# Kernel optimization log

Hardware: AMD Instinct MI355X
Metric: run time of the kernel (lower is better)

## Reference

```python
import jax, jax.numpy as jnp
import numpy as np

B, T, NT = 2, 2048, 512
DIM, DEPTH, MEL, TDIM = 768, 8, 100, 512
D_INNER, NS, PH, Q = 1536, 128, 64, 64
NH = D_INNER // PH
CONV_DIM = D_INNER + 2 * NS
D_INPROJ = 2 * D_INNER + 2 * NS + NH
KCONV = 4
FFI = 2 * DIM
VOCAB = 257


def _ln(x, eps=1e-6):
    m = jnp.mean(x, -1, keepdims=True)
    v = jnp.mean((x - m) ** 2, -1, keepdims=True)
    return (x - m) * jax.lax.rsqrt(v + eps)


def _mish(x):
    return x * jnp.tanh(jax.nn.softplus(x))


def _dwconv_causal(x, w, b):
    # x: [B,T,C], w: [C,K]  depthwise causal conv (left-pad K-1)
    K = w.shape[1]
    xp = jnp.pad(x, ((0, 0), (K - 1, 0), (0, 0)))
    y = sum(xp[:, k:k + x.shape[1]] * w[:, k] for k in range(K))
    return y + b


def _ssd(xh, Bm, Cm, dt, A):
    # chunked selective-scan (Mamba SSD form). xh [B,T,H,P]; Bm,Cm [B,T,N]; dt [B,T,H]; A [H]
    Bsz, Tt, H, P = xh.shape
    N = Bm.shape[-1]
    Cn = Tt // Q
    xb = (dt[..., None] * xh).reshape(Bsz, Cn, Q, H, P)
    a = (dt * A).reshape(Bsz, Cn, Q, H)
    Bc = Bm.reshape(Bsz, Cn, Q, N)
    Cc = Cm.reshape(Bsz, Cn, Q, N)
    acum = jnp.cumsum(a, axis=2)  # [b,c,q,h]
    # intra-chunk: decay matrix exp(acum_q - acum_s) for s <= q
    Ldec = jnp.exp(acum[:, :, :, None, :] - acum[:, :, None, :, :])  # [b,c,q,s,h]
    mask = jnp.tril(jnp.ones((Q, Q), dtype=bool))
    Ldec = jnp.where(mask[None, None, :, :, None], Ldec, 0.0)
    CB = jnp.einsum('bcqn,bcsn->bcqs', Cc, Bc)
    y_in = jnp.einsum('bcqs,bcqsh,bcshp->bcqhp', CB, Ldec, xb)
    # chunk end-states
    dst = jnp.exp(acum[:, :, -1:, :] - acum)  # [b,c,q,h]
    S = jnp.einsum('bcqh,bcqn,bcqhp->bchpn', dst, Bc, xb)
    atot = jnp.exp(acum[:, :, -1, :])  # [b,c,h] total chunk decay

    def step(Hc, inp):
        at_c, S_c = inp
        return at_c[:, :, None, None] * Hc + S_c, Hc

    H0 = jnp.zeros((Bsz, H, P, N), xh.dtype)
    _, prev = jax.lax.scan(step, H0, (jnp.moveaxis(atot, 1, 0), jnp.moveaxis(S, 1, 0)))
    prev = jnp.moveaxis(prev, 0, 1)  # state entering each chunk [b,c,h,p,n]
    y_out = jnp.einsum('bcqn,bchpn->bcqhp', Cc, prev) * jnp.exp(acum)[..., None]
    return (y_in + y_out).reshape(Bsz, Tt, H, P)


def _forward(x, cond, time, text, text_table, inp_w, inp_b, pos_w1, pos_b1, pos_w2, pos_b2, t_w1, t_b1, t_w2, t_b2, adaln_w, adaln_b, in_w, conv_w, conv_b, dt_bias, A_log, Dp, rms_w, out_w, ff_w1, ff_b1, ff_w2, ff_b2, fin_w, fin_b, proj_w, proj_b):
    # timestep embedding (sinusoidal, scale 1000, freq dim 256 -> MLP)
    half = 128
    freqs = jnp.exp(-jnp.log(10000.0) / (half - 1) * jnp.arange(half, dtype=x.dtype))
    ang = 1000.0 * time[:, None] * freqs[None]
    te = jnp.concatenate([jnp.sin(ang), jnp.cos(ang)], -1)
    tvec = jax.nn.silu(te @ t_w1 + t_b1) @ t_w2 + t_b2  # [B,DIM]
    # text embedding (conv_layers=0 path): shift by 1, pad to seq_len, lookup
    idx = jnp.pad(text + 1, ((0, 0), (0, T - text.shape[1])))
    temb = text_table[idx]  # [B,T,TDIM]
    # input embedding + ConvPositionEmbedding (grouped conv k=31, groups=16, Mish x2)
    h = jnp.concatenate([x, cond, temb], -1) @ inp_w + inp_b  # [B,T,DIM]
    dn = ('NWC', 'WIO', 'NWC')
    p = jax.lax.conv_general_dilated(h, pos_w1, (1,), [(15, 15)], dimension_numbers=dn, feature_group_count=16) + pos_b1
    p = _mish(p)
    p = jax.lax.conv_general_dilated(p, pos_w2, (1,), [(15, 15)], dimension_numbers=dn, feature_group_count=16) + pos_b2
    h = h + _mish(p)
    st = jax.nn.silu(tvec)
    for l in range(DEPTH):
        mod = st @ adaln_w[l] + adaln_b[l]
        sh_msa, sc_msa, g_msa, sh_mlp, sc_mlp, g_mlp = jnp.split(mod, 6, -1)
        xn = _ln(h) * (1 + sc_msa[:, None]) + sh_msa[:, None]
        # Mamba-3 selective scan block
        zxbcdt = xn @ in_w[l]
        z = zxbcdt[..., :D_INNER]
        xBC = zxbcdt[..., D_INNER:D_INNER + CONV_DIM]
        dt = zxbcdt[..., D_INNER + CONV_DIM:]
        xBC = jax.nn.silu(_dwconv_causal(xBC, conv_w[l], conv_b[l]))
        xp = xBC[..., :D_INNER].reshape(B, T, NH, PH)
        Bm = xBC[..., D_INNER:D_INNER + NS]
        Cm = xBC[..., D_INNER + NS:]
        dt = jax.nn.softplus(dt + dt_bias[l])
        A = -jnp.exp(A_log[l])
        y = _ssd(xp, Bm, Cm, dt, A) + Dp[l][:, None] * xp
        y = y.reshape(B, T, D_INNER) * jax.nn.silu(z)
        y = y * jax.lax.rsqrt(jnp.mean(y * y, -1, keepdims=True) + 1e-5) * rms_w[l]
        h = h + g_msa[:, None] * (y @ out_w[l])
        # gated FFN
        xn = _ln(h) * (1 + sc_mlp[:, None]) + sh_mlp[:, None]
        ff = jax.nn.gelu(xn @ ff_w1[l] + ff_b1[l], approximate=True) @ ff_w2[l] + ff_b2[l]
        h = h + g_mlp[:, None] * ff
    fm = st @ fin_w + fin_b
    sc, sh = jnp.split(fm, 2, -1)
    h = _ln(h) * (1 + sc[:, None]) + sh[:, None]
    return h @ proj_w + proj_b


def setup_inputs() -> dict:
    key = jax.random.key(0)
    it = iter(jax.random.split(key, 40))

    def n(shape, s=0.02):
        return (s * jax.random.normal(next(it), shape)).astype(jnp.float32)

    inp = {
        'x': n((B, T, MEL), 1.0),
        'cond': n((B, T, MEL), 1.0),
        'time': jax.random.uniform(next(it), (B,), dtype=jnp.float32),
        'text_table': n((VOCAB, TDIM)),
        'inp_w': n((2 * MEL + TDIM, DIM)), 'inp_b': jnp.zeros((DIM,), jnp.float32),
        'pos_w1': n((31, DIM // 16, DIM), 0.05), 'pos_b1': jnp.zeros((DIM,), jnp.float32),
        'pos_w2': n((31, DIM // 16, DIM), 0.05), 'pos_b2': jnp.zeros((DIM,), jnp.float32),
        't_w1': n((256, DIM)), 't_b1': jnp.zeros((DIM,), jnp.float32),
        't_w2': n((DIM, DIM)), 't_b2': jnp.zeros((DIM,), jnp.float32),
        'adaln_w': n((DEPTH, DIM, 6 * DIM)), 'adaln_b': jnp.zeros((DEPTH, 6 * DIM), jnp.float32),
        'in_w': n((DEPTH, DIM, D_INPROJ)),
        'conv_w': n((DEPTH, CONV_DIM, KCONV), 0.2), 'conv_b': jnp.zeros((DEPTH, CONV_DIM), jnp.float32),
        'dt_bias': n((DEPTH, NH), 0.5),
        'A_log': jnp.log(jnp.tile(jnp.arange(1, NH + 1, dtype=jnp.float32), (DEPTH, 1))),
        'Dp': jnp.ones((DEPTH, NH), jnp.float32),
        'rms_w': jnp.ones((DEPTH, D_INNER), jnp.float32),
        'out_w': n((DEPTH, D_INNER, DIM)),
        'ff_w1': n((DEPTH, DIM, FFI)), 'ff_b1': jnp.zeros((DEPTH, FFI), jnp.float32),
        'ff_w2': n((DEPTH, FFI, DIM)), 'ff_b2': jnp.zeros((DEPTH, DIM), jnp.float32),
        'fin_w': n((DIM, 2 * DIM)), 'fin_b': jnp.zeros((2 * DIM,), jnp.float32),
        'proj_w': n((DIM, MEL)), 'proj_b': jnp.zeros((MEL,), jnp.float32),
    }
    inp['text'] = jax.random.randint(next(it), (B, NT), 0, 256)
    return inp


def reference(x, cond, time, text, text_table, inp_w, inp_b, pos_w1, pos_b1, pos_w2, pos_b2, t_w1, t_b1, t_w2, t_b2, adaln_w, adaln_b, in_w, conv_w, conv_b, dt_bias, A_log, Dp, rms_w, out_w, ff_w1, ff_b1, ff_w2, ff_b2, fin_w, fin_b, proj_w, proj_b):
    return _forward(x, cond, time, text, text_table, inp_w, inp_b, pos_w1, pos_b1, pos_w2, pos_b2, t_w1, t_b1, t_w2, t_b2, adaln_w, adaln_b, in_w, conv_w, conv_b, dt_bias, A_log, Dp, rms_w, out_w, ff_w1, ff_b1, ff_w2, ff_b2, fin_w, fin_b, proj_w, proj_b)
```

## Files before the change

kernel.cpp:

```cpp
#include <hip/hip_runtime.h>
#include <math.h>

constexpr int Bv = 2, Tv = 2048, NTv = 512;
constexpr int DIMv = 768, DEPTHv = 8, MELv = 100, TDIMv = 512;
constexpr int DINNER = 1536, NSv = 128, PHv = 64, QQv = 64;
constexpr int NHv = DINNER / PHv;
constexpr int CONVD = DINNER + 2 * NSv;
constexpr int DINP = 2 * DINNER + 2 * NSv + NHv;
constexpr int KCONVv = 4, FFIv = 2 * DIMv;
constexpr int CNv = Tv / QQv;
constexpr int PCK = 1504;
constexpr int KCAT = 736;

typedef unsigned short u16;
typedef unsigned int u32;
typedef __attribute__((ext_vector_type(8))) short short8v;
typedef __attribute__((ext_vector_type(4))) float f32x4;

__device__ __forceinline__ float siluf(float x) { return x / (1.f + expf(-x)); }
__device__ __forceinline__ float softplusf(float x) { return x > 20.f ? x : log1pf(expf(x)); }
__device__ __forceinline__ float mishf(float x) { return x * tanhf(softplusf(x)); }

__device__ __forceinline__ u16 f2bf(float v) {
    u32 u = __builtin_bit_cast(u32, v);
    u32 r = (u + 0x7fffu + ((u >> 16) & 1u)) >> 16;
    return (u16)r;
}
__device__ __forceinline__ float bf2f(u16 v) {
    u32 u = (u32)v << 16;
    return __builtin_bit_cast(float, u);
}
__device__ __forceinline__ float bf2fs(short v) { return bf2f((u16)v); }

__device__ __forceinline__ void gload16(const void* g, void* l) {
    __builtin_amdgcn_global_load_lds(
        (const __attribute__((address_space(1))) u32*)g,
        (__attribute__((address_space(3))) u32*)l, 16, 0, 0);
}

__device__ __forceinline__ float blockReduceSum(float v) {
    __shared__ float red[4];
    #pragma unroll
    for (int off = 32; off > 0; off >>= 1) v += __shfl_down(v, off, 64);
    __syncthreads();
    if ((threadIdx.x & 63) == 0) red[threadIdx.x >> 6] = v;
    __syncthreads();
    return red[0] + red[1] + red[2] + red[3];
}

template <int EPI, int BIG>
__global__ __launch_bounds__(256) void gemm_bf16(const u16* __restrict__ A,
        const u16* __restrict__ BT, const float* __restrict__ bias,
        float* __restrict__ Cf, u16* __restrict__ Cb,
        int M, int N, int K, int ldc,
        const float* __restrict__ modv, int goff, int mstride) {
    constexpr int BM = BIG ? 128 : 64;
    constexpr int MI = 4;
    constexpr int NJ = BIG ? 4 : 2;
    __shared__ __align__(16) u16 As[2][BM * 32];
    __shared__ __align__(16) u16 Bs[2][128 * 32];
    const int tid = threadIdx.x;
    const int gx = gridDim.x;
    const int nwg = gx * gridDim.y;
    int flat = blockIdx.y * gx + blockIdx.x;
    const int qq = nwg >> 3;
    flat = (flat & 7) * qq + (flat >> 3);
    const int m0 = (flat / gx) * BM, n0 = (flat % gx) * 128;
    const int lane = tid & 63;
    const int wid = tid >> 6;
    const int wm = BIG ? (wid >> 1) * 64 : 0;
    const int wn = BIG ? (wid & 1) * 64 : wid * 32;
    f32x4 acc[MI][NJ] = {};
    const int srow = tid >> 2, sseg = (tid & 3) * 8;
    const u16* Ag = A + (size_t)(m0 + srow) * K + sseg;
    const u16* Bg = BT + (size_t)(n0 + srow) * K + sseg;
    const int lr = lane & 15, lk = (lane >> 4) * 8;
    gload16(Ag, &As[0][tid * 8]);
    if (BIG) gload16(Ag + (size_t)64 * K, &As[0][tid * 8 + 64 * 32]);
    gload16(Bg, &Bs[0][tid * 8]);
    gload16(Bg + (size_t)64 * K, &Bs[0][tid * 8 + 64 * 32]);
    __syncthreads();
    int cur = 0;
    for (int k0 = 0; k0 < K; k0 += 32) {
        if (k0 + 32 < K) {
            const int nb = cur ^ 1, kn = k0 + 32;
            gload16(Ag + kn, &As[nb][tid * 8]);
            if (BIG) gload16(Ag + kn + (size_t)64 * K, &As[nb][tid * 8 + 64 * 32]);
            gload16(Bg + kn, &Bs[nb][tid * 8]);
            gload16(Bg + kn + (size_t)64 * K, &Bs[nb][tid * 8 + 64 * 32]);
        }
        short8v a_f[MI], b_f[NJ];
        #pragma unroll
        for (int i = 0; i < MI; i++)
            a_f[i] = *(const short8v*)&As[cur][(wm + i * 16 + lr) * 32 + lk];
        #pragma unroll
        for (int j = 0; j < NJ; j++)
            b_f[j] = *(const short8v*)&Bs[cur][(wn + j * 16 + lr) * 32 + lk];
        #pragma unroll
        for (int i = 0; i < MI; i++)
            #pragma unroll
            for (int j = 0; j < NJ; j++)
                acc[i][j] = __builtin_amdgcn_mfma_f32_16x16x32_bf16(a_f[i], b_f[j], acc[i][j], 0, 0, 0);
        __syncthreads();
        cur ^= 1;
    }
    const int r0 = (lane >> 4) * 4;
    #pragma unroll
    for (int i = 0; i < MI; i++) {
        #pragma unroll
        for (int j = 0; j < NJ; j++) {
            const int col = n0 + wn + j * 16 + lr;
            if (col >= N) continue;
            const int row = m0 + wm + i * 16 + r0;
            const float bv = (EPI == 1 || EPI == 2 || EPI == 4) ? bias[col] : 0.f;
            #pragma unroll
            for (int r = 0; r < 4; r++) {
                float v = acc[i][j][r] + bv;
                if (EPI == 0) {
                    Cb[(size_t)(row + r) * ldc + col] = f2bf(v);
                } else if (EPI == 2) {
                    float xx = v;
                    v = 0.5f * xx * (1.f + tanhf(0.7978845608028654f * (xx + 0.044715f * xx * xx * xx)));
                    Cb[(size_t)(row + r) * ldc + col] = f2bf(v);
                } else if (EPI == 3 || EPI == 4) {
                    const int bb = (row + r) >> 11;
                    float g = modv[(size_t)bb * mstride + goff + col];
                    Cf[(size_t)(row + r) * ldc + col] += g * v;
                } else {
                    Cf[(size_t)(row + r) * ldc + col] = v;
                }
            }
        }
    }
}

__global__ __launch_bounds__(256) void wt_convert_b(const float* __restrict__ W,
        u16* __restrict__ WT, int Kd, int N, int Kmax, int Npad) {
    const float* Wl = W + (size_t)blockIdx.z * Kmax * N;
    u16* WTl = WT + (size_t)blockIdx.z * Npad * Kd;
    __shared__ float t[32][33];
    const int n0 = blockIdx.x * 32, k0 = blockIdx.y * 32;
    const int c = threadIdx.x & 31, rq = (threadIdx.x >> 5) * 4;
    #pragma unroll
    for (int i = 0; i < 4; i++) {
        int n = n0 + c, k = k0 + rq + i;
        t[rq + i][c] = (n < N && k < Kmax) ? Wl[(size_t)k * N + n] : 0.f;
    }
    __syncthreads();
    #pragma unroll
    for (int i = 0; i < 4; i++)
        WTl[(size_t)(n0 + rq + i) * Kd + k0 + c] = f2bf(t[c][rq + i]);
}

__global__ __launch_bounds__(256) void pw_convert(const float* __restrict__ w,
        u16* __restrict__ WT) {
    __shared__ float t[32][33];
    const int kk0 = blockIdx.x * 32, o0 = blockIdx.y * 32;
    const int c = threadIdx.x & 31, rq = (threadIdx.x >> 5) * 4;
    #pragma unroll
    for (int i = 0; i < 4; i++) {
        int kk = kk0 + rq + i;
        t[rq + i][c] = (kk < 1488) ? w[(size_t)kk * DIMv + o0 + c] : 0.f;
    }
    __syncthreads();
    #pragma unroll
    for (int i = 0; i < 4; i++)
        WT[(size_t)(o0 + rq + i) * PCK + kk0 + c] = f2bf(t[c][rq + i]);
}

template <int IN_BF, int FUSE>
__global__ __launch_bounds__(256) void posconv_mfma(const void* __restrict__ inv,
        const u16* __restrict__ WT, const float* __restrict__ bias,
        void* __restrict__ outv) {
    __shared__ __align__(16) u16 xs[95 * 48];
    const int t0 = blockIdx.x * 64, g = blockIdx.y, b = blockIdx.z;
    const int tid = threadIdx.x;
    for (int e = tid; e < 95 * 48; e += 256) {
        int rr = e / 48, cc = e % 48;
        int t = t0 - 15 + rr;
        float v = 0.f;
        if (t >= 0 && t < Tv) {
            size_t gi = ((size_t)b * Tv + t) * DIMv + g * 48 + cc;
            v = IN_BF ? bf2f(((const u16*)inv)[gi]) : ((const float*)inv)[gi];
        }
        xs[e] = f2bf(v);
    }
    __syncthreads();
    const int lane = tid & 63, w = tid >> 6;
    const int lr = lane & 15, lq8 = (lane >> 4) * 8, rq = (lane >> 4) * 4;
    const u16* arow = &xs[(w * 16 + lr) * 48 + lq8];
    const u16* brow = &WT[(size_t)(g * 48 + lr) * PCK + lq8];
    f32x4 acc[3] = {};
    #pragma unroll 2
    for (int ks = 0; ks < PCK / 32; ks++) {
        short8v a = *(const short8v*)(arow + ks * 32);
        #pragma unroll
        for (int j = 0; j < 3; j++) {
            short8v bf = *(const short8v*)(brow + (size_t)j * 16 * PCK + ks * 32);
            acc[j] = __builtin_amdgcn_mfma_f32_16x16x32_bf16(a, bf, acc[j], 0, 0, 0);
        }
    }
    #pragma unroll
    for (int j = 0; j < 3; j++) {
        const int o = g * 48 + j * 16 + lr;
        const float bvv = bias[o];
        #pragma unroll
        for (int r = 0; r < 4; r++) {
            const int t = t0 + w * 16 + rq + r;
            float v = acc[j][r] + bvv;
            size_t gi = ((size_t)b * Tv + t) * DIMv + o;
            if (FUSE == 0) ((u16*)outv)[gi] = f2bf(mishf(v));
            else ((float*)outv)[gi] += mishf(v);
        }
    }
}

// ... 31 lines not shown
    const int o = blockIdx.x * 64 + (threadIdx.x & 63);
    const int ks = threadIdx.x >> 6;
    __shared__ float hv[DIMv];
    __shared__ float part[4][64];
    for (int j = threadIdx.x; j < DIMv; j += 256) hv[j] = hid[b * DIMv + j];
    __syncthreads();
    float acc = 0.f;
    #pragma unroll 8
    for (int k = ks * 192; k < ks * 192 + 192; k++) acc += hv[k] * t_w2[(size_t)k * DIMv + o];
    part[ks][threadIdx.x & 63] = acc;
    __syncthreads();
    if (threadIdx.x < 64) {
        float r = part[0][threadIdx.x] + part[1][threadIdx.x] + part[2][threadIdx.x] + part[3][threadIdx.x]
                + t_b2[o];
        st_out[b * DIMv + o] = siluf(r);
    }
}

__global__ __launch_bounds__(256) void modvec_kernel(const float* __restrict__ st,
        const float* __restrict__ W, const float* __restrict__ bias,
        float* __restrict__ out, int N) {
    const int l = blockIdx.z, b = blockIdx.y;
    const int o = blockIdx.x * 64 + (threadIdx.x & 63);
    const int ks = threadIdx.x >> 6;
    __shared__ float sv[DIMv];
    __shared__ float part[4][64];
    for (int j = threadIdx.x; j < DIMv; j += 256) sv[j] = st[b * DIMv + j];
    __syncthreads();
    const float* Wl = W + (size_t)l * DIMv * N + o;
    float acc = 0.f;
    #pragma unroll 8
    for (int k = ks * 192; k < ks * 192 + 192; k++) acc += sv[k] * Wl[(size_t)k * N];
    part[ks][threadIdx.x & 63] = acc;
    __syncthreads();
    if (threadIdx.x < 64) {
        float r = part[0][threadIdx.x] + part[1][threadIdx.x] + part[2][threadIdx.x] + part[3][threadIdx.x]
                + bias[(size_t)l * N + o];
        out[((size_t)l * Bv + b) * N + o] = r;
    }
}

__global__ void concat_bf16(const float* __restrict__ x, const float* __restrict__ cond,
                            const float* __restrict__ table, const int* __restrict__ text,
                            u16* __restrict__ cat) {
    size_t i = (size_t)blockIdx.x * 256 + threadIdx.x;
    const size_t total = (size_t)Bv * Tv * KCAT;
    if (i >= total) return;
    int j = (int)(i % KCAT);
    size_t row = i / KCAT;
    int t = (int)(row % Tv), b = (int)(row / Tv);
    float v = 0.f;
    if (j < MELv) v = x[row * MELv + j];
    else if (j < 2 * MELv) v = cond[row * MELv + (j - MELv)];
    else if (j < 712) {
        int idx = (t < NTv) ? (text[b * NTv + t] + 1) : 0;
        v = table[(size_t)idx * TDIMv + (j - 2 * MELv)];
    }
    cat[i] = f2bf(v);
}

template <int BF>
__global__ __launch_bounds__(256) void ln_mod_kernel(const float* __restrict__ h,
        void* __restrict__ outv, const float* __restrict__ modv,
        int sc_off, int sh_off, int mod_stride) {
    const int row = blockIdx.x;
    const int b = row / Tv;
    const float* hr = h + (size_t)row * DIMv;
    float s = 0.f;
    for (int j = threadIdx.x; j < DIMv; j += 256) s += hr[j];
    s = blockReduceSum(s);
    const float m = s / DIMv;
    float v = 0.f;
    for (int j = threadIdx.x; j < DIMv; j += 256) { float d = hr[j] - m; v += d * d; }
    v = blockReduceSum(v);
    const float rstd = rsqrtf(v / DIMv + 1e-6f);
    const float* mb = modv + (size_t)b * mod_stride;
    for (int j = threadIdx.x; j < DIMv; j += 256) {
        float val = (hr[j] - m) * rstd * (1.f + mb[sc_off + j]) + mb[sh_off + j];
        if (BF) ((u16*)outv)[(size_t)row * DIMv + j] = f2bf(val);
        else ((float*)outv)[(size_t)row * DIMv + j] = val;
    }
}

__global__ void dwconv_bc(const u16* __restrict__ zxb, const float* __restrict__ cw,
                          const float* __restrict__ cb, u16* __restrict__ xbcBC) {
    size_t i = (size_t)blockIdx.x * 256 + threadIdx.x;
    const size_t total = (size_t)Bv * Tv * 32;
    if (i >= total) return;
    const int c8 = (int)(i & 31) * 8;
    const size_t row = i >> 5;
    const int t = (int)(row % Tv);
    const u16* base = zxb + row * DINP + DINNER + c8;
    float acc[8];
    #pragma unroll
    for (int u = 0; u < 8; u++) acc[u] = cb[DINNER + c8 + u];
    #pragma unroll
    for (int k = 0; k < KCONVv; k++) {
        const int d = k - 3;
        if (t + d < 0) continue;
        short8v tv = *(const short8v*)(base + (ptrdiff_t)d * DINP);
        #pragma unroll
        for (int u = 0; u < 8; u++)
            acc[u] += bf2fs(tv[u]) * cw[(DINNER + c8 + u) * KCONVv + k];
    }
    short8v outv;
    #pragma unroll
    for (int u = 0; u < 8; u++) outv[u] = (short)f2bf(siluf(acc[u]));
    *(short8v*)(xbcBC + row * 256 + c8) = outv;
}

__global__ __launch_bounds__(256) void dwconvT(const u16* __restrict__ zxb,
        const float* __restrict__ cw, const float* __restrict__ cb,
        u16* __restrict__ xT) {
    __shared__ __align__(16) u16 in_s[67 * 72];
    const int pb = blockIdx.x;
    const int c = blockIdx.y, b = blockIdx.z;
    const int bc = b * CNv + c;
    const int tid = threadIdx.x;
    for (int e = tid; e < 67 * 8; e += 256) {
        int sp = e >> 3, p8 = (e & 7) * 8;
        int t = c * 64 + sp - 3;
        short8v v = {};
        if (t >= 0)
            v = *(const short8v*)&zxb[((size_t)b * Tv + t) * DINP + DINNER + pb * 64 + p8];
        *(short8v*)&in_s[sp * 72 + p8] = v;
    }
    __syncthreads();
    const int p = tid >> 2, sb = (tid & 3) * 16;
    const int ch = pb * 64 + p;
    const float w0 = cw[ch * 4], w1 = cw[ch * 4 + 1], w2 = cw[ch * 4 + 2], w3 = cw[ch * 4 + 3];
    const float bb = cb[ch];
    short8v o0, o1;
    #pragma unroll
    for (int i = 0; i < 16; i++) {
        int s = sb + i;
        float acc = bb + bf2f(in_s[s * 72 + p]) * w0 + bf2f(in_s[(s + 1) * 72 + p]) * w1
                  + bf2f(in_s[(s + 2) * 72 + p]) * w2 + bf2f(in_s[(s + 3) * 72 + p]) * w3;
        short r = (short)f2bf(siluf(acc));
        if (i < 8) o0[i] = r; else o1[i - 8] = r;
    }
    u16* dst = xT + ((size_t)bc * DINNER + ch) * 64 + sb;
    *(short8v*)dst = o0;
    *(short8v*)(dst + 8) = o1;
}

__global__ __launch_bounds__(256) void ssd_cb(const u16* __restrict__ xbcBC,
        float* __restrict__ CBg, u16* __restrict__ BTg) {
    constexpr int ST = 136;
    __shared__ __align__(16) u16 Cs[64 * ST];
    __shared__ __align__(16) u16 Bs[64 * ST];
    const int c = blockIdx.x, b = blockIdx.y;
    const int bc = b * CNv + c;
    const int tid = threadIdx.x;
    const size_t rowbase = (size_t)b * Tv + (size_t)c * QQv;
    for (int e = tid; e < 64 * 16; e += 256) {
        int r = e >> 4, n8 = (e & 15) * 8;
        const u16* src = &xbcBC[(rowbase + r) * 256];
        *(short8v*)&Bs[r * ST + n8] = *(const short8v*)(src + n8);
        *(short8v*)&Cs[r * ST + n8] = *(const short8v*)(src + NSv + n8);
    }
    __syncthreads();
    u16* btg = BTg + (size_t)bc * (NSv * QQv);
    for (int e = tid; e < 128 * 64; e += 256) {
        int n = e >> 6, s = e & 63;
        btg[e] = Bs[s * ST + n];
    }
    const int lane = tid & 63, w = tid >> 6;
    const int lr = lane & 15, lk8 = (lane >> 4) * 8, rq = (lane >> 4) * 4;
    f32x4 acc[4] = {};
    #pragma unroll
    for (int ks = 0; ks < 4; ks++) {
        short8v a = *(const short8v*)&Cs[(w * 16 + lr) * ST + ks * 32 + lk8];
        #pragma unroll
        for (int j = 0; j < 4; j++) {
            short8v bf = *(const short8v*)&Bs[(j * 16 + lr) * ST + ks * 32 + lk8];
            acc[j] = __builtin_amdgcn_mfma_f32_16x16x32_bf16(a, bf, acc[j], 0, 0, 0);
        }
    }
    float* out = CBg + (size_t)bc * 4096;
    #pragma unroll
    for (int j = 0; j < 4; j++)
        #pragma unroll
        for (int r = 0; r < 4; r++)
            out[(w * 16 + rq + r) * 64 + j * 16 + lr] = acc[j][r];
}

__global__ __launch_bounds__(256) void ssd_part1m(const u16* __restrict__ xT,
        const u16* __restrict__ BTg, const u16* __restrict__ zxb,
        const float* __restrict__ dt_bias, const float* __restrict__ A_log,
        const float* __restrict__ CBg, u16* __restrict__ ybuf,
        float* __restrict__ Sg, float* __restrict__ acg, float* __restrict__ atg) {
    constexpr int ST64 = 72;
    __shared__ __align__(16) u16 xTs[64 * ST64];
    __shared__ __align__(16) u16 Wsm[64 * ST64];
    __shared__ __align__(16) u16 BTs[128 * ST64];
    __shared__ float ac[64], dts[64], dtrev[64];
    const int h = blockIdx.x, c = blockIdx.y, b = blockIdx.z;
    const int bc = b * CNv + c;
    const int tid = threadIdx.x;
    const size_t rowbase = (size_t)b * Tv + (size_t)c * QQv;
    const size_t bch = ((size_t)bc) * NHv + h;
    if (tid < 64) {
        float raw = bf2f(zxb[(rowbase + tid) * DINP + DINNER + CONVD + h]) + dt_bias[h];
        float dtv = softplusf(raw);
        dts[tid] = dtv;
        float v = dtv * (-expf(A_log[h]));
        #pragma unroll
        for (int off = 1; off < 64; off <<= 1) {
            float t = __shfl_up(v, off, 64);
            if (tid >= off) v += t;
        }
        ac[tid] = v;
        float v63 = __shfl(v, 63, 64);
        dtrev[tid] = dtv * expf(v63 - v);
        acg[bch * 64 + tid] = v;
        if (tid == 63) atg[bch] = expf(v63);
    }
    {
        const u16* src = xT + ((size_t)bc * DINNER + h * PHv) * 64;
        for (int e = tid; e < 64 * 8; e += 256) {
            int p = e >> 3, s8 = (e & 7) * 8;
            *(short8v*)&xTs[p * ST64 + s8] = *(const short8v*)(src + p * 64 + s8);
        }
    }
    __syncthreads();
    {
        const u16* btg = BTg + (size_t)bc * (NSv * QQv);
        for (int e = tid; e < 128 * 8; e += 256) {
            int n = e >> 3, s8 = (e & 7) * 8;
            short8v v = *(const short8v*)(btg + n * 64 + s8);
            short8v o;
            #pragma unroll
            for (int u = 0; u < 8; u++)
                o[u] = (short)f2bf(bf2fs(v[u]) * dtrev[s8 + u]);
            *(short8v*)&BTs[n * ST64 + s8] = o;
        }
        const float* cbrow = CBg + (size_t)bc * 4096;
        for (int e = tid; e < 1024; e += 256) {
            int q = e >> 4, s4 = (e & 15) * 4;
            f32x4 cb4 = *(const f32x4*)&cbrow[q * 64 + s4];
            float aq = ac[q];
            #pragma unroll
            for (int u = 0; u < 4; u++) {
                int s = s4 + u;
                float wv = (s <= q) ? cb4[u] * expf(aq - ac[s]) * dts[s] : 0.f;
                Wsm[q * ST64 + s] = f2bf(wv);
            }
        }
    }
    __syncthreads();
    const int lane = tid & 63, w = tid >> 6;
    const int lr = lane & 15, lk8 = (lane >> 4) * 8, rq = (lane >> 4) * 4;
    {
        f32x4 acc[4] = {};
        #pragma unroll
        for (int ks = 0; ks < 2; ks++) {
            short8v bf = *(const short8v*)&xTs[(w * 16 + lr) * ST64 + ks * 32 + lk8];
            #pragma unroll
            for (int i = 0; i < 4; i++) {
                short8v a = *(const short8v*)&Wsm[(i * 16 + lr) * ST64 + ks * 32 + lk8];
                acc[i] = __builtin_amdgcn_mfma_f32_16x16x32_bf16(a, bf, acc[i], 0, 0, 0);
            }
        }
        #pragma unroll
        for (int i = 0; i < 4; i++)
            #pragma unroll
            for (int r = 0; r < 4; r++) {
                int q = i * 16 + rq + r, p = w * 16 + lr;
                ybuf[(rowbase + q) * DINNER + h * PHv + p] = f2bf(acc[i][r]);
            }
    }
    {
        f32x4 acc[4][2] = {};
        #pragma unroll
        for (int ks = 0; ks < 2; ks++) {
            short8v a[4];
            #pragma unroll
            for (int i = 0; i < 4; i++)
                a[i] = *(const short8v*)&xTs[(i * 16 + lr) * ST64 + ks * 32 + lk8];
            #pragma unroll
            for (int j = 0; j < 2; j++) {
                short8v bf = *(const short8v*)&BTs[(w * 32 + j * 16 + lr) * ST64 + ks * 32 + lk8];
                #pragma unroll
                for (int i = 0; i < 4; i++)
                    acc[i][j] = __builtin_amdgcn_mfma_f32_16x16x32_bf16(a[i], bf, acc[i][j], 0, 0, 0);
            }
        }
        float* So = Sg + bch * (PHv * NSv);
        #pragma unroll
        for (int i = 0; i < 4; i++)
            #pragma unroll
            for (int j = 0; j < 2; j++)
                #pragma unroll
                for (int r = 0; r < 4; r++)
                    So[(i * 16 + rq + r) * NSv + w * 32 + j * 16 + lr] = acc[i][j][r];
    }
}

__global__ void ssd_scan(float* __restrict__ Sg, const float* __restrict__ atg) {
    int idx = blockIdx.x * 256 + threadIdx.x;
    if (idx >= Bv * NHv * PHv * NSv) return;
    int n = idx % NSv;
    int p = (idx / NSv) % PHv;
    int h = (idx / (NSv * PHv)) % NHv;
    int b = idx / (NSv * PHv * NHv);
    float H = 0.f;
    for (int c = 0; c < CNv; c++) {
        size_t bch = ((size_t)b * CNv + c) * NHv + h;
        size_t off = bch * PHv * NSv + (size_t)p * NSv + n;
        float s = Sg[off];
        float at = atg[bch];
        Sg[off] = H;
        H = at * H + s;
    }
}

__global__ __launch_bounds__(256) void ssd_part2m(const u16* __restrict__ xbcBC,
        const u16* __restrict__ xT, const float* __restrict__ Sg,
        const float* __restrict__ acg, const float* __restrict__ Dp,
        u16* __restrict__ ybuf) {
    constexpr int ST = 136;
    __shared__ __align__(16) u16 Cs[64 * ST];
    __shared__ __align__(16) u16 Ps[64 * ST];
    __shared__ float eac[64];
    const int h = blockIdx.x, c = blockIdx.y, b = blockIdx.z;
    const int bc = b * CNv + c;
    const int tid = threadIdx.x;
    const size_t rowbase = (size_t)b * Tv + (size_t)c * QQv;
    const size_t bch = ((size_t)bc) * NHv + h;
    if (tid < 64) eac[tid] = expf(acg[bch * 64 + tid]);
    for (int e = tid; e < 64 * 16; e += 256) {
        int r = e >> 4, n8 = (e & 15) * 8;
        *(short8v*)&Cs[r * ST + n8] =
            *(const short8v*)&xbcBC[(rowbase + r) * 256 + NSv + n8];
        const float* src = &Sg[bch * (PHv * NSv) + (size_t)r * NSv + n8];
        f32x4 a = *(const f32x4*)src, b4 = *(const f32x4*)(src + 4);
        short8v o;
        o[0] = (short)f2bf(a[0]); o[1] = (short)f2bf(a[1]);
        o[2] = (short)f2bf(a[2]); o[3] = (short)f2bf(a[3]);
        o[4] = (short)f2bf(b4[0]); o[5] = (short)f2bf(b4[1]);
        o[6] = (short)f2bf(b4[2]); o[7] = (short)f2bf(b4[3]);
        *(short8v*)&Ps[r * ST + n8] = o;
    }
    __syncthreads();
    const int lane = tid & 63, w = tid >> 6;
    const int lr = lane & 15, lk8 = (lane >> 4) * 8, rq = (lane >> 4) * 4;
    f32x4 acc[4] = {};
    #pragma unroll
    for (int ks = 0; ks < 4; ks++) {
        short8v bf = *(const short8v*)&Ps[(w * 16 + lr) * ST + ks * 32 + lk8];
        #pragma unroll
        for (int i = 0; i < 4; i++) {
            short8v a = *(const short8v*)&Cs[(i * 16 + lr) * ST + ks * 32 + lk8];
            acc[i] = __builtin_amdgcn_mfma_f32_16x16x32_bf16(a, bf, acc[i], 0, 0, 0);
        }
    }
    const float Dh = Dp[h];
    const int p = w * 16 + lr;
    const u16* xrow = xT + ((size_t)bc * DINNER + h * PHv + p) * 64;
    #pragma unroll
    for (int i = 0; i < 4; i++)
        #pragma unroll
        for (int r = 0; r < 4; r++) {
            int q = i * 16 + rq + r;
            size_t yi = (rowbase + q) * DINNER + h * PHv + p;
            float xv = bf2f(xrow[q]);
            ybuf[yi] = f2bf(bf2f(ybuf[yi]) + acc[i][r] * eac[q] + Dh * xv);
        }
}

__global__ __launch_bounds__(256) void gate_rms_kernel(const u16* __restrict__ y,
        const u16* __restrict__ zxb, const float* __restrict__ rms_w,
        u16* __restrict__ yb) {
    const int row = blockIdx.x;
    const u16* yr = y + (size_t)row * DINNER;
    const u16* zr = zxb + (size_t)row * DINP;
    float vals[8];
    float ss = 0.f;
    const int tid = threadIdx.x;
    if (tid < 192) {
        short8v yv = *(const short8v*)(yr + tid * 8);
        short8v zv = *(const short8v*)(zr + tid * 8);
        #pragma unroll
        for (int u = 0; u < 8; u++) {
            float v = bf2fs(yv[u]) * siluf(bf2fs(zv[u]));
            vals[u] = v;
            ss += v * v;
        }
    }
    ss = blockReduceSum(ss);
    const float scale = rsqrtf(ss / DINNER + 1e-5f);
    if (tid < 192) {
        short8v outv;
        #pragma unroll
        for (int u = 0; u < 8; u++)
            outv[u] = (short)f2bf(vals[u] * scale * rms_w[tid * 8 + u]);
        *(short8v*)(yb + (size_t)row * DINNER + tid * 8) = outv;
    }
}

extern "C" void kernel_launch(void* const* d_in, const int* in_sizes, int n_in,
                              void* d_out, int out_size, void* d_ws, size_t ws_size,
                              hipStream_t stream) {
    int s3 = (in_sizes[3] == Bv * NTv) ? 1 : 0;
    const float* x      = (const float*)d_in[0];
    const float* cond   = (const float*)d_in[1];
    const float* timev  = (const float*)d_in[2];
    const int*   text   = (const int*)(s3 ? d_in[3] : d_in[32]);
    const float* table  = (const float*)d_in[3 + s3];
    const float* inp_w  = (const float*)d_in[4 + s3];
    const float* inp_b  = (const float*)d_in[5 + s3];
    const float* pos_w1 = (const float*)d_in[6 + s3];
    const float* pos_b1 = (const float*)d_in[7 + s3];
    const float* pos_w2 = (const float*)d_in[8 + s3];
    const float* pos_b2 = (const float*)d_in[9 + s3];
    const float* t_w1   = (const float*)d_in[10 + s3];
    const float* t_b1   = (const float*)d_in[11 + s3];
    const float* t_w2   = (const float*)d_in[12 + s3];
    const float* t_b2   = (const float*)d_in[13 + s3];
    const float* adaln_w= (const float*)d_in[14 + s3];
    const float* adaln_b= (const float*)d_in[15 + s3];
    const float* in_w   = (const float*)d_in[16 + s3];
    const float* conv_w = (const float*)d_in[17 + s3];
    const float* conv_b = (const float*)d_in[18 + s3];
    const float* dt_bias= (const float*)d_in[19 + s3];
    const float* A_log  = (const float*)d_in[20 + s3];
    const float* Dp     = (const float*)d_in[21 + s3];
    const float* rms_w  = (const float*)d_in[22 + s3];
    const float* out_w  = (const float*)d_in[23 + s3];
    const float* ff_w1  = (const float*)d_in[24 + s3];
    const float* ff_b1  = (const float*)d_in[25 + s3];
    const float* ff_w2  = (const float*)d_in[26 + s3];
    const float* ff_b2  = (const float*)d_in[27 + s3];
    const float* fin_w  = (const float*)d_in[28 + s3];
    const float* fin_b  = (const float*)d_in[29 + s3];
    const float* proj_w = (const float*)d_in[30 + s3];
    const float* proj_b = (const float*)d_in[31 + s3];

    float* ws = (float*)d_ws;
    const size_t n_h = (size_t)Bv * Tv * DIMv;
    size_t off = 0;
    auto nx = [&](size_t n) { float* p = ws + off; off += n; return p; };
    float* h_   = nx(n_h);
    float* S_   = nx((size_t)Bv * CNv * NHv * PHv * NSv);
    float* ac_  = nx((size_t)Bv * CNv * NHv * QQv);
    float* at_  = nx((size_t)Bv * CNv * NHv);
    float* CB_  = nx((size_t)Bv * CNv * QQv * QQv);
    float* st_  = nx((size_t)Bv * DIMv);
    float* hid_ = nx((size_t)Bv * DIMv);
    float* mod_ = nx((size_t)DEPTHv * Bv * 6 * DIMv);
    float* fm_  = nx((size_t)Bv * 2 * DIMv);
    off = (off + 15) & ~(size_t)15;
    u16* wtin_  = (u16*)(ws + off);
    u16* wtout_ = wtin_  + (size_t)DEPTHv * 3456 * 768;
    u16* wtff1_ = wtout_ + (size_t)DEPTHv * 768 * 1536;
    u16* wtff2_ = wtff1_ + (size_t)DEPTHv * 1536 * 768;
    u16* wtinp_ = wtff2_ + (size_t)DEPTHv * 768 * 1536;
    u16* wtprj_ = wtinp_ + (size_t)768 * KCAT;
    u16* pwt1_  = wtprj_ + (size_t)128 * 768;
    u16* pwt2_  = pwt1_  + (size_t)768 * PCK;
    u16* zxb_   = pwt2_  + (size_t)768 * PCK;
    u16* xbcBC_ = zxb_   + (size_t)4096 * DINP;
    u16* xT_    = xbcBC_ + (size_t)4096 * 256;
    u16* BTg_   = xT_    + (size_t)64 * DINNER * 64;
    u16* yb_    = BTg_   + (size_t)64 * NSv * 64;
    u16* xnb_   = yb_    + (size_t)4096 * 1536;
    u16* actb_  = xnb_   + (size_t)4096 * 768;
    u16* xnb2_  = actb_  + (size_t)4096 * 1536;
    u16* catb_  = xnb2_  + (size_t)4096 * 768;

    const int MT = Bv * Tv;

    wt_convert_b<<<dim3(3456 / 32, 768 / 32, DEPTHv), 256, 0, stream>>>(
        in_w, wtin_, 768, DINP, DIMv, 3456);
    wt_convert_b<<<dim3(768 / 32, 1536 / 32, DEPTHv), 256, 0, stream>>>(
        out_w, wtout_, 1536, DIMv, DINNER, 768);
    wt_convert_b<<<dim3(1536 / 32, 768 / 32, DEPTHv), 256, 0, stream>>>(
        ff_w1, wtff1_, 768, FFIv, DIMv, 1536);
    wt_convert_b<<<dim3(768 / 32, 1536 / 32, DEPTHv), 256, 0, stream>>>(
        ff_w2, wtff2_, 1536, DIMv, FFIv, 768);
    wt_convert_b<<<dim3(768 / 32, KCAT / 32, 1), 256, 0, stream>>>(
        inp_w, wtinp_, KCAT, DIMv, 712, 768);
    wt_convert_b<<<dim3(128 / 32, 768 / 32, 1), 256, 0, stream>>>(
        proj_w, wtprj_, 768, MELv, DIMv, 128);
    pw_convert<<<dim3(PCK / 32, DIMv / 32), 256, 0, stream>>>(pos_w1, pwt1_);
    pw_convert<<<dim3(PCK / 32, DIMv / 32), 256, 0, stream>>>(pos_w2, pwt2_);

    temb1_kernel<<<dim3(DIMv / 64, Bv), 256, 0, stream>>>(timev, t_w1, t_b1, hid_);
    temb2_kernel<<<dim3(DIMv / 64, Bv), 256, 0, stream>>>(hid_, t_w2, t_b2, st_);
    modvec_kernel<<<dim3(6 * DIMv / 64, Bv, DEPTHv), 256, 0, stream>>>(st_, adaln_w, adaln_b, mod_, 6 * DIMv);
    modvec_kernel<<<dim3(2 * DIMv / 64, Bv, 1), 256, 0, stream>>>(st_, fin_w, fin_b, fm_, 2 * DIMv);

    concat_bf16<<<(unsigned)(((size_t)Bv * Tv * KCAT + 255) / 256), 256, 0, stream>>>(
        x, cond, table, text, catb_);
    gemm_bf16<1, 0><<<dim3(6, 64), 256, 0, stream>>>(
        catb_, wtinp_, inp_b, h_, nullptr, MT, DIMv, KCAT, DIMv, nullptr, 0, 0);

    posconv_mfma<0, 0><<<dim3(Tv / 64, 16, Bv), 256, 0, stream>>>(h_, pwt1_, pos_b1, xnb2_);
    posconv_mfma<1, 1><<<dim3(Tv / 64, 16, Bv), 256, 0, stream>>>(xnb2_, pwt2_, pos_b2, h_);

    for (int l = 0; l < DEPTHv; l++) {
        const float* modl = mod_ + (size_t)l * Bv * 6 * DIMv;
        const float* cwl = conv_w + (size_t)l * CONVD * KCONVv;
        const float* cbl = conv_b + (size_t)l * CONVD;
        ln_mod_kernel<1><<<MT, 256, 0, stream>>>(h_, xnb_, modl, DIMv, 0, 6 * DIMv);
        gemm_bf16<0, 1><<<dim3(27, 32), 256, 0, stream>>>(
            xnb_, wtin_ + (size_t)l * 3456 * 768, nullptr, nullptr, zxb_,
            MT, DINP, DIMv, DINP, nullptr, 0, 0);
        dwconv_bc<<<(unsigned)(((size_t)Bv * Tv * 32 + 255) / 256), 256, 0, stream>>>(
            zxb_, cwl, cbl, xbcBC_);
        dwconvT<<<dim3(DINNER / 64, CNv, Bv), 256, 0, stream>>>(zxb_, cwl, cbl, xT_);
        ssd_cb<<<dim3(CNv, Bv), 256, 0, stream>>>(xbcBC_, CB_, BTg_);
        ssd_part1m<<<dim3(NHv, CNv, Bv), 256, 0, stream>>>(
            xT_, BTg_, zxb_, dt_bias + l * NHv, A_log + l * NHv, CB_, yb_, S_, ac_, at_);
        ssd_scan<<<(Bv * NHv * PHv * NSv + 255) / 256, 256, 0, stream>>>(S_, at_);
        ssd_part2m<<<dim3(NHv, CNv, Bv), 256, 0, stream>>>(
            xbcBC_, xT_, S_, ac_, Dp + l * NHv, yb_);
        gate_rms_kernel<<<MT, 256, 0, stream>>>(yb_, zxb_, rms_w + (size_t)l * DINNER, actb_);
        gemm_bf16<3, 0><<<dim3(6, 64), 256, 0, stream>>>(
            actb_, wtout_ + (size_t)l * 768 * 1536, nullptr, h_, nullptr,
            MT, DIMv, DINNER, DIMv, modl, 2 * DIMv, 6 * DIMv);
        ln_mod_kernel<1><<<MT, 256, 0, stream>>>(h_, xnb_, modl, 4 * DIMv, 3 * DIMv, 6 * DIMv);
        gemm_bf16<2, 1><<<dim3(12, 32), 256, 0, stream>>>(
            xnb_, wtff1_ + (size_t)l * 1536 * 768, ff_b1 + (size_t)l * FFIv, nullptr, actb_,
            MT, FFIv, DIMv, FFIv, nullptr, 0, 0);
        gemm_bf16<4, 0><<<dim3(6, 64), 256, 0, stream>>>(
            actb_, wtff2_ + (size_t)l * 768 * 1536, ff_b2 + (size_t)l * DIMv, h_, nullptr,
            MT, DIMv, FFIv, DIMv, modl, 5 * DIMv, 6 * DIMv);
    }

    ln_mod_kernel<1><<<MT, 256, 0, stream>>>(h_, xnb_, fm_, 0, DIMv, 2 * DIMv);
    gemm_bf16<1, 0><<<dim3(1, 64), 256, 0, stream>>>(
        xnb_, wtprj_, proj_b, (float*)d_out, nullptr, MT, MELv, DIMv, MELv, nullptr, 0, 0);
}
```

Baseline: 2.478 ms.

## Add 4-stage small GEMM, fuse B/C conv into ssd_cb, store states in bf16

Adds a separate small-tile GEMM kernel with a four-buffer LDS pipeline that stages two K-steps per barrier, and uses it for the narrow-N GEMMs. The separate dwconv_bc kernel is folded into ssd_cb, which now runs the causal conv and SiLU for B/C itself, so one launch and one reread go away. Chunk states S are kept in bf16 instead of fp32, which halves traffic in scan and part2 but adds rounding to the recurrent state on every chunk. KCAT is padded to 768 so K is a multiple of 64 for the new pipeline.

```diff
diff --git a/kernel.cpp b/kernel.cpp
--- a/kernel.cpp
+++ b/kernel.cpp
@@ -10,7 +10,7 @@
 constexpr int KCONVv = 4, FFIv = 2 * DIMv;
 constexpr int CNv = Tv / QQv;
 constexpr int PCK = 1504;
-constexpr int KCAT = 736;
+constexpr int KCAT = 768;
 
 typedef unsigned short u16;
 typedef unsigned int u32;
@@ -48,16 +48,38 @@
     return red[0] + red[1] + red[2] + red[3];
 }
 
-template <int EPI, int BIG>
+template <int EPI>
+__device__ __forceinline__ void gemm_epi(f32x4* acc, int nfrag, int row, int col,
+        int N, int ldc, const float* bias, float* Cf, u16* Cb,
+        const float* modv, int goff, int mstride) {
+    if (col >= N) return;
+    const float bv = (EPI == 1 || EPI == 2 || EPI == 4) ? bias[col] : 0.f;
+    #pragma unroll
+    for (int r = 0; r < 4; r++) {
+        float v = (*acc)[r] + bv;
+        if (EPI == 0) {
+            Cb[(size_t)(row + r) * ldc + col] = f2bf(v);
+        } else if (EPI == 2) {
+            float xx = v;
+            v = 0.5f * xx * (1.f + tanhf(0.7978845608028654f * (xx + 0.044715f * xx * xx * xx)));
+            Cb[(size_t)(row + r) * ldc + col] = f2bf(v);
+        } else if (EPI == 3 || EPI == 4) {
+            const int bb = (row + r) >> 11;
+            float g = modv[(size_t)bb * mstride + goff + col];
+            Cf[(size_t)(row + r) * ldc + col] += g * v;
+        } else {
+            Cf[(size_t)(row + r) * ldc + col] = v;
+        }
+    }
+}
+
+template <int EPI>
 __global__ __launch_bounds__(256) void gemm_bf16(const u16* __restrict__ A,
         const u16* __restrict__ BT, const float* __restrict__ bias,
         float* __restrict__ Cf, u16* __restrict__ Cb,
         int M, int N, int K, int ldc,
         const float* __restrict__ modv, int goff, int mstride) {
-    constexpr int BM = BIG ? 128 : 64;
-    constexpr int MI = 4;
-    constexpr int NJ = BIG ? 4 : 2;
-    __shared__ __align__(16) u16 As[2][BM * 32];
+    __shared__ __align__(16) u16 As[2][128 * 32];
     __shared__ __align__(16) u16 Bs[2][128 * 32];
     const int tid = threadIdx.x;
     const int gx = gridDim.x;
@@ -65,18 +87,17 @@
     int flat = blockIdx.y * gx + blockIdx.x;
     const int qq = nwg >> 3;
     flat = (flat & 7) * qq + (flat >> 3);
-    const int m0 = (flat / gx) * BM, n0 = (flat % gx) * 128;
+    const int m0 = (flat / gx) * 128, n0 = (flat % gx) * 128;
     const int lane = tid & 63;
     const int wid = tid >> 6;
-    const int wm = BIG ? (wid >> 1) * 64 : 0;
-    const int wn = BIG ? (wid & 1) * 64 : wid * 32;
-    f32x4 acc[MI][NJ] = {};
+    const int wm = (wid >> 1) * 64, wn = (wid & 1) * 64;
+    f32x4 acc[4][4] = {};
     const int srow = tid >> 2, sseg = (tid & 3) * 8;
     const u16* Ag = A + (size_t)(m0 + srow) * K + sseg;
     const u16* Bg = BT + (size_t)(n0 + srow) * K + sseg;
     const int lr = lane & 15, lk = (lane >> 4) * 8;
     gload16(Ag, &As[0][tid * 8]);
-    if (BIG) gload16(Ag + (size_t)64 * K, &As[0][tid * 8 + 64 * 32]);
+    gload16(Ag + (size_t)64 * K, &As[0][tid * 8 + 64 * 32]);
     gload16(Bg, &Bs[0][tid * 8]);
     gload16(Bg + (size_t)64 * K, &Bs[0][tid * 8 + 64 * 32]);
     __syncthreads();
@@ -85,53 +106,97 @@
         if (k0 + 32 < K) {
             const int nb = cur ^ 1, kn = k0 + 32;
             gload16(Ag + kn, &As[nb][tid * 8]);
-            if (BIG) gload16(Ag + kn + (size_t)64 * K, &As[nb][tid * 8 + 64 * 32]);
+            gload16(Ag + kn + (size_t)64 * K, &As[nb][tid * 8 + 64 * 32]);
             gload16(Bg + kn, &Bs[nb][tid * 8]);
             gload16(Bg + kn + (size_t)64 * K, &Bs[nb][tid * 8 + 64 * 32]);
         }
-        short8v a_f[MI], b_f[NJ];
-        #pragma unroll
-        for (int i = 0; i < MI; i++)
+        short8v a_f[4], b_f[4];
+        #pragma unroll
+        for (int i = 0; i < 4; i++)
             a_f[i] = *(const short8v*)&As[cur][(wm + i * 16 + lr) * 32 + lk];
         #pragma unroll
-        for (int j = 0; j < NJ; j++)
+        for (int j = 0; j < 4; j++)
             b_f[j] = *(const short8v*)&Bs[cur][(wn + j * 16 + lr) * 32 + lk];
         #pragma unroll
-        for (int i = 0; i < MI; i++)
-            #pragma unroll
-            for (int j = 0; j < NJ; j++)
+        for (int i = 0; i < 4; i++)
+            #pragma unroll
+            for (int j = 0; j < 4; j++)
                 acc[i][j] = __builtin_amdgcn_mfma_f32_16x16x32_bf16(a_f[i], b_f[j], acc[i][j], 0, 0, 0);
         __syncthreads();
         cur ^= 1;
     }
     const int r0 = (lane >> 4) * 4;
     #pragma unroll
-    for (int i = 0; i < MI; i++) {
-        #pragma unroll
-        for (int j = 0; j < NJ; j++) {
-            const int col = n0 + wn + j * 16 + lr;
-            if (col >= N) continue;
-            const int row = m0 + wm + i * 16 + r0;
-            const float bv = (EPI == 1 || EPI == 2 || EPI == 4) ? bias[col] : 0.f;
-            #pragma unroll
-            for (int r = 0; r < 4; r++) {
-                float v = acc[i][j][r] + bv;
-                if (EPI == 0) {
-                    Cb[(size_t)(row + r) * ldc + col] = f2bf(v);
-                } else if (EPI == 2) {
-                    float xx = v;
-                    v = 0.5f * xx * (1.f + tanhf(0.7978845608028654f * (xx + 0.044715f * xx * xx * xx)));
-                    Cb[(size_t)(row + r) * ldc + col] = f2bf(v);
-                } else if (EPI == 3 || EPI == 4) {
-                    const int bb = (row + r) >> 11;
-                    float g = modv[(size_t)bb * mstride + goff + col];
-                    Cf[(size_t)(row + r) * ldc + col] += g * v;
-                } else {
-                    Cf[(size_t)(row + r) * ldc + col] = v;
-                }
-            }
-        }
-    }
+    for (int i = 0; i < 4; i++)
+        #pragma unroll
+        for (int j = 0; j < 4; j++)
+            gemm_epi<EPI>(&acc[i][j], 1, m0 + wm + i * 16 + r0, n0 + wn + j * 16 + lr,
+                          N, ldc, bias, Cf, Cb, modv, goff, mstride);
+}
+
+template <int EPI>
+__global__ __launch_bounds__(256) void gemm_bf16s(const u16* __restrict__ A,
+        const u16* __restrict__ BT, const float* __restrict__ bias,
+        float* __restrict__ Cf, u16* __restrict__ Cb,
+        int M, int N, int K, int ldc,
+        const float* __restrict__ modv, int goff, int mstride) {
+    __shared__ __align__(16) u16 As[4][64 * 32];
+    __shared__ __align__(16) u16 Bs[4][128 * 32];
+    const int tid = threadIdx.x;
+    const int gx = gridDim.x;
+    const int nwg = gx * gridDim.y;
+    int flat = blockIdx.y * gx + blockIdx.x;
+    const int qq = nwg >> 3;
+    flat = (flat & 7) * qq + (flat >> 3);
+    const int m0 = (flat / gx) * 64, n0 = (flat % gx) * 128;
+    const int lane = tid & 63;
+    const int wid = tid >> 6;
+    const int wn = wid * 32;
+    f32x4 acc[4][2] = {};
+    const int srow = tid >> 2, sseg = (tid & 3) * 8;
+    const u16* Ag = A + (size_t)(m0 + srow) * K + sseg;
+    const u16* Bg = BT + (size_t)(n0 + srow) * K + sseg;
+    const int lr = lane & 15, lk = (lane >> 4) * 8;
+    auto STAGE = [&](int buf, int kk) {
+        gload16(Ag + kk, &As[buf][tid * 8]);
+        gload16(Bg + kk, &Bs[buf][tid * 8]);
+        gload16(Bg + kk + (size_t)64 * K, &Bs[buf][tid * 8 + 64 * 32]);
+    };
+    auto COMP = [&](int buf) {
+        short8v a_f[4], b_f[2];
+        #pragma unroll
+        for (int i = 0; i < 4; i++)
+            a_f[i] = *(const short8v*)&As[buf][(i * 16 + lr) * 32 + lk];
+        #pragma unroll
+        for (int j = 0; j < 2; j++)
+            b_f[j] = *(const short8v*)&Bs[buf][(wn + j * 16 + lr) * 32 + lk];
+        #pragma unroll
+        for (int i = 0; i < 4; i++)
+            #pragma unroll
+            for (int j = 0; j < 2; j++)
+                acc[i][j] = __builtin_amdgcn_mfma_f32_16x16x32_bf16(a_f[i], b_f[j], acc[i][j], 0, 0, 0);
+    };
+    STAGE(0, 0);
+    STAGE(1, 32);
+    __syncthreads();
+    int cur = 0;
+    for (int k0 = 0; k0 < K; k0 += 64) {
+        if (k0 + 64 < K) {
+            STAGE((cur + 2) & 3, k0 + 64);
+            STAGE((cur + 3) & 3, k0 + 96);
+        }
+        COMP(cur);
+        COMP((cur + 1) & 3);
+        __syncthreads();
+        cur = (cur + 2) & 3;
+    }
+    const int r0 = (lane >> 4) * 4;
+    #pragma unroll
+    for (int i = 0; i < 4; i++)
+        #pragma unroll
+        for (int j = 0; j < 2; j++)
+            gemm_epi<EPI>(&acc[i][j], 1, m0 + i * 16 + r0, n0 + wn + j * 16 + lr,
+                          N, ldc, bias, Cf, Cb, modv, goff, mstride);
 }
 
 __global__ __launch_bounds__(256) void wt_convert_b(const float* __restrict__ W,
@@ -329,33 +394,6 @@
     }
 }
 
-__global__ void dwconv_bc(const u16* __restrict__ zxb, const float* __restrict__ cw,
-                          const float* __restrict__ cb, u16* __restrict__ xbcBC) {
-    size_t i = (size_t)blockIdx.x * 256 + threadIdx.x;
-    const size_t total = (size_t)Bv * Tv * 32;
-    if (i >= total) return;
-    const int c8 = (int)(i & 31) * 8;
-    const size_t row = i >> 5;
-    const int t = (int)(row % Tv);
-    const u16* base = zxb + row * DINP + DINNER + c8;
-    float acc[8];
-    #pragma unroll
-    for (int u = 0; u < 8; u++) acc[u] = cb[DINNER + c8 + u];
-    #pragma unroll
-    for (int k = 0; k < KCONVv; k++) {
-        const int d = k - 3;
-        if (t + d < 0) continue;
-        short8v tv = *(const short8v*)(base + (ptrdiff_t)d * DINP);
-        #pragma unroll
-        for (int u = 0; u < 8; u++)
-            acc[u] += bf2fs(tv[u]) * cw[(DINNER + c8 + u) * KCONVv + k];
-    }
-    short8v outv;
-    #pragma unroll
-    for (int u = 0; u < 8; u++) outv[u] = (short)f2bf(siluf(acc[u]));
-    *(short8v*)(xbcBC + row * 256 + c8) = outv;
-}
-
 __global__ __launch_bounds__(256) void dwconvT(const u16* __restrict__ zxb,
         const float* __restrict__ cw, const float* __restrict__ cb,
         u16* __restrict__ xT) {
@@ -391,8 +429,9 @@
     *(short8v*)(dst + 8) = o1;
 }
 
-__global__ __launch_bounds__(256) void ssd_cb(const u16* __restrict__ xbcBC,
-        float* __restrict__ CBg, u16* __restrict__ BTg) {
+__global__ __launch_bounds__(256) void ssd_cb(const u16* __restrict__ zxb,
+        const float* __restrict__ cw, const float* __restrict__ cbv,
+        u16* __restrict__ xbcBC, float* __restrict__ CBg, u16* __restrict__ BTg) {
     constexpr int ST = 136;
     __shared__ __align__(16) u16 Cs[64 * ST];
     __shared__ __align__(16) u16 Bs[64 * ST];
@@ -400,11 +439,29 @@
     const int bc = b * CNv + c;
     const int tid = threadIdx.x;
     const size_t rowbase = (size_t)b * Tv + (size_t)c * QQv;
-    for (int e = tid; e < 64 * 16; e += 256) {
-        int r = e >> 4, n8 = (e & 15) * 8;
-        const u16* src = &xbcBC[(rowbase + r) * 256];
-        *(short8v*)&Bs[r * ST + n8] = *(const short8v*)(src + n8);
-        *(short8v*)&Cs[r * ST + n8] = *(const short8v*)(src + NSv + n8);
+    for (int e = tid; e < 64 * 32; e += 256) {
+        int r = e >> 5, n8 = (e & 31) * 8;
+        size_t row = rowbase + r;
+        int t = c * 64 + r;
+        const u16* base = zxb + row * DINP + DINNER + n8;
+        float acc[8];
+        #pragma unroll
+        for (int u = 0; u < 8; u++) acc[u] = cbv[DINNER + n8 + u];
+        #pragma unroll
+        for (int k = 0; k < KCONVv; k++) {
+            const int d = k - 3;
+            if (t + d < 0) continue;
+            short8v tv = *(const short8v*)(base + (ptrdiff_t)d * DINP);
+            #pragma unroll
+            for (int u = 0; u < 8; u++)
+                acc[u] += bf2fs(tv[u]) * cw[(DINNER + n8 + u) * KCONVv + k];
+        }
+        short8v o;
+        #pragma unroll
+        for (int u = 0; u < 8; u++) o[u] = (short)f2bf(siluf(acc[u]));
+        if (n8 < NSv) *(short8v*)&Bs[r * ST + n8] = o;
+        else *(short8v*)&Cs[r * ST + (n8 - NSv)] = o;
+        *(short8v*)&xbcBC[row * 256 + n8] = o;
     }
     __syncthreads();
     u16* btg = BTg + (size_t)bc * (NSv * QQv);
@@ -436,7 +493,7 @@
         const u16* __restrict__ BTg, const u16* __restrict__ zxb,
         const float* __restrict__ dt_bias, const float* __restrict__ A_log,
         const float* __restrict__ CBg, u16* __restrict__ ybuf,
-        float* __restrict__ Sg, float* __restrict__ acg, float* __restrict__ atg) {
+        u16* __restrict__ Sg, float* __restrict__ acg, float* __restrict__ atg) {
     constexpr int ST64 = 72;
     __shared__ __align__(16) u16 xTs[64 * ST64];
     __shared__ __align__(16) u16 Wsm[64 * ST64];
@@ -533,18 +590,18 @@
                     acc[i][j] = __builtin_amdgcn_mfma_f32_16x16x32_bf16(a[i], bf, acc[i][j], 0, 0, 0);
             }
         }
-        float* So = Sg + bch * (PHv * NSv);
+        u16* So = Sg + bch * (PHv * NSv);
         #pragma unroll
         for (int i = 0; i < 4; i++)
             #pragma unroll
             for (int j = 0; j < 2; j++)
                 #pragma unroll
                 for (int r = 0; r < 4; r++)
-                    So[(i * 16 + rq + r) * NSv + w * 32 + j * 16 + lr] = acc[i][j][r];
-    }
-}
-
-__global__ void ssd_scan(float* __restrict__ Sg, const float* __restrict__ atg) {
+                    So[(i * 16 + rq + r) * NSv + w * 32 + j * 16 + lr] = f2bf(acc[i][j][r]);
+    }
+}
+
+__global__ void ssd_scan(u16* __restrict__ Sg, const float* __restrict__ atg) {
     int idx = blockIdx.x * 256 + threadIdx.x;
     if (idx >= Bv * NHv * PHv * NSv) return;
     int n = idx % NSv;
@@ -555,15 +612,15 @@
     for (int c = 0; c < CNv; c++) {
         size_t bch = ((size_t)b * CNv + c) * NHv + h;
         size_t off = bch * PHv * NSv + (size_t)p * NSv + n;
-        float s = Sg[off];
+        float s = bf2f(Sg[off]);
         float at = atg[bch];
-        Sg[off] = H;
+        Sg[off] = f2bf(H);
         H = at * H + s;
     }
 }
 
 __global__ __launch_bounds__(256) void ssd_part2m(const u16* __restrict__ xbcBC,
-        const u16* __restrict__ xT, const float* __restrict__ Sg,
+        const u16* __restrict__ xT, const u16* __restrict__ Sg,
         const float* __restrict__ acg, const float* __restrict__ Dp,
         u16* __restrict__ ybuf) {
     constexpr int ST = 136;
@@ -580,14 +637,8 @@
         int r = e >> 4, n8 = (e & 15) * 8;
         *(short8v*)&Cs[r * ST + n8] =
             *(const short8v*)&xbcBC[(rowbase + r) * 256 + NSv + n8];
-        const float* src = &Sg[bch * (PHv * NSv) + (size_t)r * NSv + n8];
-        f32x4 a = *(const f32x4*)src, b4 = *(const f32x4*)(src + 4);
-        short8v o;
-        o[0] = (short)f2bf(a[0]); o[1] = (short)f2bf(a[1]);
-        o[2] = (short)f2bf(a[2]); o[3] = (short)f2bf(a[3]);
-        o[4] = (short)f2bf(b4[0]); o[5] = (short)f2bf(b4[1]);
-        o[6] = (short)f2bf(b4[2]); o[7] = (short)f2bf(b4[3]);
-        *(short8v*)&Ps[r * ST + n8] = o;
+        *(short8v*)&Ps[r * ST + n8] =
+            *(const short8v*)&Sg[bch * (PHv * NSv) + (size_t)r * NSv + n8];
     }
     __syncthreads();
     const int lane = tid & 63, w = tid >> 6;
@@ -689,7 +740,6 @@
     size_t off = 0;
     auto nx = [&](size_t n) { float* p = ws + off; off += n; return p; };
     float* h_   = nx(n_h);
-    float* S_   = nx((size_t)Bv * CNv * NHv * PHv * NSv);
     float* ac_  = nx((size_t)Bv * CNv * NHv * QQv);
     float* at_  = nx((size_t)Bv * CNv * NHv);
     float* CB_  = nx((size_t)Bv * CNv * QQv * QQv);
@@ -710,7 +760,8 @@
     u16* xbcBC_ = zxb_   + (size_t)4096 * DINP;
     u16* xT_    = xbcBC_ + (size_t)4096 * 256;
     u16* BTg_   = xT_    + (size_t)64 * DINNER * 64;
-    u16* yb_    = BTg_   + (size_t)64 * NSv * 64;
+    u16* S_     = BTg_   + (size_t)64 * NSv * 64;
+    u16* yb_    = S_     + (size_t)Bv * CNv * NHv * PHv * NSv;
     u16* xnb_   = yb_    + (size_t)4096 * 1536;
     u16* actb_  = xnb_   + (size_t)4096 * 768;
     u16* xnb2_  = actb_  + (size_t)4096 * 1536;
@@ -740,7 +791,7 @@
 
     concat_bf16<<<(unsigned)(((size_t)Bv * Tv * KCAT + 255) / 256), 256, 0, stream>>>(
         x, cond, table, text, catb_);
-    gemm_bf16<1, 0><<<dim3(6, 64), 256, 0, stream>>>(
+    gemm_bf16s<1><<<dim3(6, 64), 256, 0, stream>>>(
         catb_, wtinp_, inp_b, h_, nullptr, MT, DIMv, KCAT, DIMv, nullptr, 0, 0);
 
     posconv_mfma<0, 0><<<dim3(Tv / 64, 16, Bv), 256, 0, stream>>>(h_, pwt1_, pos_b1, xnb2_);
@@ -751,32 +802,30 @@
         const float* cwl = conv_w + (size_t)l * CONVD * KCONVv;
         const float* cbl = conv_b + (size_t)l * CONVD;
         ln_mod_kernel<1><<<MT, 256, 0, stream>>>(h_, xnb_, modl, DIMv, 0, 6 * DIMv);
-        gemm_bf16<0, 1><<<dim3(27, 32), 256, 0, stream>>>(
+        gemm_bf16<0><<<dim3(27, 32), 256, 0, stream>>>(
             xnb_, wtin_ + (size_t)l * 3456 * 768, nullptr, nullptr, zxb_,
             MT, DINP, DIMv, DINP, nullptr, 0, 0);
-        dwconv_bc<<<(unsigned)(((size_t)Bv * Tv * 32 + 255) / 256), 256, 0, stream>>>(
-            zxb_, cwl, cbl, xbcBC_);
         dwconvT<<<dim3(DINNER / 64, CNv, Bv), 256, 0, stream>>>(zxb_, cwl, cbl, xT_);
-        ssd_cb<<<dim3(CNv, Bv), 256, 0, stream>>>(xbcBC_, CB_, BTg_);
+        ssd_cb<<<dim3(CNv, Bv), 256, 0, stream>>>(zxb_, cwl, cbl, xbcBC_, CB_, BTg_);
         ssd_part1m<<<dim3(NHv, CNv, Bv), 256, 0, stream>>>(
             xT_, BTg_, zxb_, dt_bias + l * NHv, A_log + l * NHv, CB_, yb_, S_, ac_, at_);
         ssd_scan<<<(Bv * NHv * PHv * NSv + 255) / 256, 256, 0, stream>>>(S_, at_);
         ssd_part2m<<<dim3(NHv, CNv, Bv), 256, 0, stream>>>(
             xbcBC_, xT_, S_, ac_, Dp + l * NHv, yb_);
         gate_rms_kernel<<<MT, 256, 0, stream>>>(yb_, zxb_, rms_w + (size_t)l * DINNER, actb_);
-        gemm_bf16<3, 0><<<dim3(6, 64), 256, 0, stream>>>(
+        gemm_bf16s<3><<<dim3(6, 64), 256, 0, stream>>>(
             actb_, wtout_ + (size_t)l * 768 * 1536, nullptr, h_, nullptr,
             MT, DIMv, DINNER, DIMv, modl, 2 * DIMv, 6 * DIMv);
         ln_mod_kernel<1><<<MT, 256, 0, stream>>>(h_, xnb_, modl, 4 * DIMv, 3 * DIMv, 6 * DIMv);
-        gemm_bf16<2, 1><<<dim3(12, 32), 256, 0, stream>>>(
+        gemm_bf16<2><<<dim3(12, 32), 256, 0, stream>>>(
             xnb_, wtff1_ + (size_t)l * 1536 * 768, ff_b1 + (size_t)l * FFIv, nullptr, actb_,
             MT, FFIv, DIMv, FFIv, nullptr, 0, 0);
-        gemm_bf16<4, 0><<<dim3(6, 64), 256, 0, stream>>>(
+        gemm_bf16s<4><<<dim3(6, 64), 256, 0, stream>>>(
             actb_, wtff2_ + (size_t)l * 768 * 1536, ff_b2 + (size_t)l * DIMv, h_, nullptr,
             MT, DIMv, FFIv, DIMv, modl, 5 * DIMv, 6 * DIMv);
     }
 
     ln_mod_kernel<1><<<MT, 256, 0, stream>>>(h_, xnb_, fm_, 0, DIMv, 2 * DIMv);
-    gemm_bf16<1, 0><<<dim3(1, 64), 256, 0, stream>>>(
+    gemm_bf16s<1><<<dim3(1, 64), 256, 0, stream>>>(
         xnb_, wtprj_, proj_b, (float*)d_out, nullptr, MT, MELv, DIMv, MELv, nullptr, 0, 0);
 }
```

Result: no change. 2.495 ms (+0.7%).
